# Performance work log

Measured on AMD Instinct MI355X. Metric: run time of the kernel, lower is better.

Reference implementation:

```python
import jax, jax.numpy as jnp
import numpy as np

B, T, D = 2, 2048, 1024
F_DIM = 4096
E = 8


def setup_inputs() -> dict:
    key = jax.random.key(0)
    ks = jax.random.split(key, 6)
    x = jax.random.normal(ks[0], (B, T, D), dtype=jnp.float32)
    Wr = jax.random.normal(ks[1], (E, D), dtype=jnp.float32) * 0.02  # router weight [E, D]
    W1 = jax.random.normal(ks[2], (E, F_DIM, D), dtype=jnp.float32) * 0.02  # per-expert Linear(D->F) weights
    b1 = jnp.zeros((E, F_DIM), dtype=jnp.float32)
    W2 = jax.random.normal(ks[3], (E, D, F_DIM), dtype=jnp.float32) * 0.02  # per-expert Linear(F->D) weights
    b2 = jnp.zeros((E, D), dtype=jnp.float32)
    return {"x": x, "Wr": Wr, "W1": W1, "b1": b1, "W2": W2, "b2": b2, "top_k": 2}


def reference(x, Wr, W1, b1, W2, b2, top_k):
    # router scores: [b, t, E]
    scores = jnp.einsum('btd,ed->bte', x, Wr)
    topk_vals, topk_idx = jax.lax.top_k(scores, top_k)  # [b, t, k]
    # Dense compute over all experts (E is small); grouped-GEMM equivalent of the
    # original per-token loop. hidden: [b, t, E, F]
    h = jax.nn.relu(jnp.einsum('btd,efd->btef', x, W1) + b1)
    all_out = jnp.einsum('btef,edf->bted', h, W2) + b2  # [b, t, E, D]
    # gather the top-k experts' outputs per token: [b, t, k, D]
    gathered = jnp.take_along_axis(all_out, topk_idx[..., None], axis=2)
    # FAITHFUL to source: softmax over the sequence dim (dim=-1 of [b, t]),
    # applied independently per top-k slot.
    weight = jax.nn.softmax(topk_vals, axis=1)  # [b, t, k]
    out = jnp.sum(weight[..., None] * gathered, axis=2)  # [b, t, D]
    return out
```

## Files before the change

kernel.cpp:

```cpp
#include <hip/hip_runtime.h>
#include <stdint.h>

typedef short bf16x8 __attribute__((ext_vector_type(8)));
typedef float f32x4 __attribute__((ext_vector_type(4)));

#define NTOK 4096
#define DDIM 1024
#define FDIM 4096
#define NEXP 8
#define SEQ  2048

#define FB_MAXROWS 8704
#define FB_MAXTILES 136
#define N_MAXROWS 9216
#define N_MAXTILES 72

#define GLOAD16(g, l) __builtin_amdgcn_global_load_lds( \
    (const __attribute__((address_space(1))) unsigned int*)(const void*)(g), \
    (__attribute__((address_space(3))) unsigned int*)(l), 16, 0, 0)

#define WAIT_LGKM0() asm volatile("s_waitcnt lgkmcnt(0)" ::: "memory")
#define WAIT_VM8()   asm volatile("s_waitcnt vmcnt(8)" ::: "memory")
#define WAIT_VM0()   asm volatile("s_waitcnt vmcnt(0)" ::: "memory")
#define SBAR()       __builtin_amdgcn_s_barrier()
#define SCHEDB()     __builtin_amdgcn_sched_barrier(0)

__device__ __forceinline__ unsigned short f2bf(float f) {
    union { float f; unsigned int u; } v; v.f = f;
    unsigned int u = v.u;
    unsigned int r = (u + 0x7FFFu + ((u >> 16) & 1u)) >> 16;
    return (unsigned short)r;
}
__device__ __forceinline__ unsigned int pk2(float a, float b) {
    return (unsigned int)f2bf(a) | ((unsigned int)f2bf(b) << 16);
}

__global__ __launch_bounds__(256) void cvt_kernel(
    const float* __restrict__ src, unsigned short* __restrict__ dst, int n4)
{
    int i = blockIdx.x * 256 + threadIdx.x;
    const int stride = gridDim.x * 256;
    for (; i < n4; i += stride) {
        const float4 v = ((const float4*)src)[i];
        ushort4 o;
        o.x = f2bf(v.x); o.y = f2bf(v.y); o.z = f2bf(v.z); o.w = f2bf(v.w);
        ((ushort4*)dst)[i] = o;
    }
}

__global__ __launch_bounds__(256) void router_kernel(
    const float* __restrict__ x, const float* __restrict__ Wr,
    float* __restrict__ topk_vals, int* __restrict__ topk_idx,
    int* __restrict__ counts)
{
    const int wave = threadIdx.x >> 6;
    const int lane = threadIdx.x & 63;
    const int t = blockIdx.x * 4 + wave;
    const float4* xr = (const float4*)(x + (size_t)t * DDIM);

    float acc[NEXP];
#pragma unroll
    for (int e = 0; e < NEXP; ++e) acc[e] = 0.0f;

    for (int d = lane; d < DDIM / 4; d += 64) {
        const float4 xv = xr[d];
#pragma unroll
        for (int e = 0; e < NEXP; ++e) {
            const float4 wv = ((const float4*)(Wr + e * DDIM))[d];
            acc[e] = fmaf(xv.x, wv.x, acc[e]);
            acc[e] = fmaf(xv.y, wv.y, acc[e]);
            acc[e] = fmaf(xv.z, wv.z, acc[e]);
            acc[e] = fmaf(xv.w, wv.w, acc[e]);
        }
    }
#pragma unroll
    for (int e = 0; e < NEXP; ++e) {
        for (int off = 32; off > 0; off >>= 1)
            acc[e] += __shfl_xor(acc[e], off, 64);
    }
    if (lane == 0) {
        float best = -3.4e38f, second = -3.4e38f;
        int bi = 0, si = 0;
#pragma unroll
        for (int e = 0; e < NEXP; ++e) {
            const float s = acc[e];
            if (s > best) { second = best; si = bi; best = s; bi = e; }
            else if (s > second) { second = s; si = e; }
        }
        topk_vals[t * 2 + 0] = best;
        topk_vals[t * 2 + 1] = second;
        topk_idx[t * 2 + 0] = bi;
        topk_idx[t * 2 + 1] = si;
        atomicAdd(&counts[bi], 1);
        atomicAdd(&counts[si], 1);
    }
}

__global__ __launch_bounds__(256) void softmax_seq_kernel(
    const float* __restrict__ tv, float* __restrict__ weight)
{
    const int b = blockIdx.x >> 1;
    const int k = blockIdx.x & 1;
    const float* base = tv + (size_t)b * SEQ * 2 + k;
    float* wbase = weight + (size_t)b * SEQ * 2 + k;
    __shared__ float red[256];
    const int tid = threadIdx.x;

    float m = -3.4e38f;
    for (int t = tid; t < SEQ; t += 256) m = fmaxf(m, base[t * 2]);
    red[tid] = m; __syncthreads();
    for (int s = 128; s > 0; s >>= 1) {
        if (tid < s) red[tid] = fmaxf(red[tid], red[tid + s]);
        __syncthreads();
    }
    m = red[0];
    __syncthreads();

    float sum = 0.0f;
    for (int t = tid; t < SEQ; t += 256) sum += expf(base[t * 2] - m);
    red[tid] = sum; __syncthreads();
    for (int s = 128; s > 0; s >>= 1) {
        if (tid < s) red[tid] += red[tid + s];
        __syncthreads();
    }
    const float inv = 1.0f / red[0];
    for (int t = tid; t < SEQ; t += 256)
        wbase[t * 2] = expf(base[t * 2] - m) * inv;
}

__global__ void scan_kernel(const int* __restrict__ counts,
                            int* __restrict__ padOff, int* __restrict__ cursor,
                            int padBits)
{
    if (threadIdx.x == 0) {
        const int pad = (1 << padBits) - 1;
        int o = 0;
        for (int e = 0; e < NEXP; ++e) {
            padOff[e] = o;
            o += ((counts[e] + pad) >> padBits) << padBits;
        }
        padOff[NEXP] = o;
    }
    if (threadIdx.x < NEXP) cursor[threadIdx.x] = 0;
}

__global__ __launch_bounds__(256) void scatter_kernel(
    const int* __restrict__ topk_idx, const int* __restrict__ padOff,
    int* __restrict__ cursor, int* __restrict__ perm)
{
    const int t = blockIdx.x * 256 + threadIdx.x;
#pragma unroll
    for (int k = 0; k < 2; ++k) {
        const int e = topk_idx[t * 2 + k];
        const int pos = padOff[e] + atomicAdd(&cursor[e], 1);
        perm[pos] = t * 2 + k;
    }
}


__global__ __launch_bounds__(256) void gemm1_p(
    const unsigned short* __restrict__ Xb, const unsigned short* __restrict__ Wb,
    const float* __restrict__ b1, const int* __restrict__ perm,
    const int* __restrict__ padOff, unsigned short* __restrict__ h)
{
    const int bid = blockIdx.x;
    const int swz = (bid & 7) * 288 + (bid >> 3);
    const int by = swz % N_MAXTILES;
    const int bx = swz / N_MAXTILES;
    const int row0 = by * 128;
    if (row0 >= padOff[NEXP]) return;
    int e = 0;
#pragma unroll
    for (int i = 1; i < NEXP; ++i) if (row0 >= padOff[i]) e = i;

    __shared__ unsigned short As[2][128 * 64];
    __shared__ unsigned short Bs[2][128 * 64];

    const int tid = threadIdx.x;
    const int w = tid >> 6, lane = tid & 63;
    const int wm = (w & 1) * 64, wn = (w >> 1) * 64;
    const int fr = lane & 15, kg = lane >> 4;
    const int col0 = bx * 128;

    const int gchunk = ((lane & 7) ^ (lane >> 3)) * 8;

    const unsigned short* aSrc[4];
    const unsigned short* bSrc[4];
#pragma unroll
    for (int j = 0; j < 4; ++j) {
        const int r = w * 32 + j * 8 + (lane >> 3);
        const int pm = perm[row0 + r];
        const int tok = (pm >= 0) ? (pm >> 1) : 0;
        aSrc[j] = Xb + (size_t)tok * DDIM + gchunk;
        bSrc[j] = Wb + ((size_t)e * FDIM + col0 + r) * DDIM + gchunk;
    }

    f32x4 acc[4][4] = {};

#define STAGE1(buf, koff) do { \
    for (int j = 0; j < 4; ++j) { \
        GLOAD16(aSrc[j] + (koff), &As[buf][(w * 4 + j) * 512]); \
        GLOAD16(bSrc[j] + (koff), &Bs[buf][(w * 4 + j) * 512]); \
    } } while (0)

    const int NT = DDIM / 64;
    STAGE1(0, 0);
    STAGE1(1, 64);
    SCHEDB(); WAIT_VM8(); SBAR(); SCHEDB();

    int cur = 0;
    for (int t = 0; t < NT; ++t) {
        const unsigned short* Ab = &As[cur][0];
        const unsigned short* Bb = &Bs[cur][0];
        bf16x8 a[2][4], b[2][4];
#pragma unroll
        for (int kk = 0; kk < 2; ++kk) {
#pragma unroll
            for (int m = 0; m < 4; ++m)
                a[kk][m] = *(const bf16x8*)&Ab[(wm + m * 16 + fr) * 64 + (((kk << 2) | kg) ^ (fr & 7)) * 8];
#pragma unroll
            for (int n = 0; n < 4; ++n)
                b[kk][n] = *(const bf16x8*)&Bb[(wn + n * 16 + fr) * 64 + (((kk << 2) | kg) ^ (fr & 7)) * 8];
        }
        WAIT_LGKM0(); SCHEDB();
        SBAR(); SCHEDB();
        if (t + 2 < NT) STAGE1(cur, (t + 2) * 64);
#pragma unroll
        for (int kk = 0; kk < 2; ++kk)
#pragma unroll
            for (int m = 0; m < 4; ++m)
#pragma unroll
                for (int n = 0; n < 4; ++n)
                    acc[m][n] = __builtin_amdgcn_mfma_f32_16x16x32_bf16(a[kk][m], b[kk][n], acc[m][n], 0, 0, 0);
        if (t + 1 < NT) {
            SCHEDB();
            if (t + 2 < NT) { WAIT_VM8(); } else { WAIT_VM0(); }
            SBAR(); SCHEDB();
        }
        cur ^= 1;
    }
#undef STAGE1

#pragma unroll
    for (int n = 0; n < 4; ++n) {
        const int colg = col0 + wn + n * 16 + fr;
        const float bias = b1[e * FDIM + colg];
#pragma unroll
        for (int m = 0; m < 4; ++m) {
#pragma unroll
            for (int r = 0; r < 4; ++r) {
                const int rowg = row0 + wm + m * 16 + kg * 4 + r;
                h[(size_t)rowg * FDIM + colg] = f2bf(fmaxf(acc[m][n][r] + bias, 0.0f));
            }
        }
    }
}

__global__ __launch_bounds__(256) void gemm2_p(
    const unsigned short* __restrict__ h, const unsigned short* __restrict__ Wb,
    const float* __restrict__ b2, const int* __restrict__ perm,
    const int* __restrict__ padOff, const float* __restrict__ weight,
    float* __restrict__ out)
{
    const int bid = blockIdx.x;
    const int swz = (bid & 7) * 144 + (bid >> 3);
    const int by = swz % N_MAXTILES;
    const int rest = swz / N_MAXTILES;
    const int bx = rest & 7;
    const int kc = rest >> 3;
    const int row0 = by * 128;
    if (row0 >= padOff[NEXP]) return;
    int e = 0;
#pragma unroll
    for (int i = 1; i < NEXP; ++i) if (row0 >= padOff[i]) e = i;

    __shared__ unsigned short As[2][128 * 64];
    __shared__ unsigned short Bs[2][128 * 64];

    const int tid = threadIdx.x;
    const int w = tid >> 6, lane = tid & 63;
    const int wm = (w & 1) * 64, wn = (w >> 1) * 64;
    const int fr = lane & 15, kg = lane >> 4;
    const int col0 = bx * 128;
    const int kbase = kc * (FDIM / 2);

    const int gchunk = ((lane & 7) ^ (lane >> 3)) * 8;

    const unsigned short* aSrc[4];
    const unsigned short* bSrc[4];
#pragma unroll
    for (int j = 0; j < 4; ++j) {
        const int r = w * 32 + j * 8 + (lane >> 3);
        aSrc[j] = h + (size_t)(row0 + r) * FDIM + kbase + gchunk;
        bSrc[j] = Wb + ((size_t)e * DDIM + col0 + r) * FDIM + kbase + gchunk;
    }

    f32x4 acc[4][4] = {};

#define STAGE2(buf, koff) do { \
    for (int j = 0; j < 4; ++j) { \
        GLOAD16(aSrc[j] + (koff), &As[buf][(w * 4 + j) * 512]); \
        GLOAD16(bSrc[j] + (koff), &Bs[buf][(w * 4 + j) * 512]); \
    } } while (0)

    const int NT = (FDIM / 2) / 64;
    STAGE2(0, 0);
    STAGE2(1, 64);
    SCHEDB(); WAIT_VM8(); SBAR(); SCHEDB();

    int cur = 0;
    for (int t = 0; t < NT; ++t) {
        const unsigned short* Ab = &As[cur][0];
        const unsigned short* Bb = &Bs[cur][0];
        bf16x8 a[2][4], b[2][4];
#pragma unroll
        for (int kk = 0; kk < 2; ++kk) {
#pragma unroll
            for (int m = 0; m < 4; ++m)
                a[kk][m] = *(const bf16x8*)&Ab[(wm + m * 16 + fr) * 64 + (((kk << 2) | kg) ^ (fr & 7)) * 8];
#pragma unroll
            for (int n = 0; n < 4; ++n)
                b[kk][n] = *(const bf16x8*)&Bb[(wn + n * 16 + fr) * 64 + (((kk << 2) | kg) ^ (fr & 7)) * 8];
        }
        WAIT_LGKM0(); SCHEDB();
        SBAR(); SCHEDB();
        if (t + 2 < NT) STAGE2(cur, (t + 2) * 64);
#pragma unroll
        for (int kk = 0; kk < 2; ++kk)
#pragma unroll
            for (int m = 0; m < 4; ++m)
#pragma unroll
                for (int n = 0; n < 4; ++n)
                    acc[m][n] = __builtin_amdgcn_mfma_f32_16x16x32_bf16(a[kk][m], b[kk][n], acc[m][n], 0, 0, 0);
        if (t + 1 < NT) {
            SCHEDB();
            if (t + 2 < NT) { WAIT_VM8(); } else { WAIT_VM0(); }
            SBAR(); SCHEDB();
        }
        cur ^= 1;
    }
#undef STAGE2

#pragma unroll
    for (int n = 0; n < 4; ++n) {
        const int colg = col0 + wn + n * 16 + fr;
        const float bias = (kc == 0) ? b2[e * DDIM + colg] : 0.0f;
#pragma unroll
        for (int m = 0; m < 4; ++m) {
#pragma unroll
            for (int r = 0; r < 4; ++r) {
                const int rowg = row0 + wm + m * 16 + kg * 4 + r;
                const int pm = perm[rowg];
                if (pm >= 0) {
                    const float wgt = weight[pm];
                    atomicAdd(&out[(size_t)(pm >> 1) * DDIM + colg], (acc[m][n][r] + bias) * wgt);
                }
            }
        }
    }
}


__global__ __launch_bounds__(256) void gemm1_fb(
    const float* __restrict__ x, const float* __restrict__ W1,
    const float* __restrict__ b1, const int* __restrict__ perm,
    const int* __restrict__ padOff, unsigned short* __restrict__ h)
{
    const int row0 = blockIdx.y * 64;
    if (row0 >= padOff[NEXP]) return;
    int e = 0;
#pragma unroll
    for (int i = 1; i < NEXP; ++i) if (row0 >= padOff[i]) e = i;

    __shared__ unsigned short As[64][40];
    __shared__ unsigned short Bs[64][40];

    const int tid = threadIdx.x;
    const int srow = tid >> 2;
    const int skp = (tid & 3) << 3;

    const int pm = perm[row0 + srow];
    const float* aSrc = (pm >= 0) ? (x + (size_t)(pm >> 1) * DDIM + skp) : 0;
    const int fRow = blockIdx.x * 64 + srow;
    const float* bSrc = W1 + ((size_t)e * FDIM + fRow) * DDIM + skp;

    const int lane = tid & 63;
    const int wm = ((tid >> 7) & 1) * 32;
    const int wn = ((tid >> 6) & 1) * 32;
    const int fr = lane & 15;
    const int kg = lane >> 4;

    f32x4 acc[2][2] = {{{0,0,0,0},{0,0,0,0}},{{0,0,0,0},{0,0,0,0}}};

    for (int k0 = 0; k0 < DDIM; k0 += 32) {
        uint4 av = make_uint4(0, 0, 0, 0);
        if (aSrc) {
            const float4 lo = *(const float4*)(aSrc + k0);
            const float4 hi = *(const float4*)(aSrc + k0 + 4);
            av.x = pk2(lo.x, lo.y); av.y = pk2(lo.z, lo.w);
            av.z = pk2(hi.x, hi.y); av.w = pk2(hi.z, hi.w);
        }
        const float4 bl = *(const float4*)(bSrc + k0);
        const float4 bh = *(const float4*)(bSrc + k0 + 4);
        uint4 bv;
        bv.x = pk2(bl.x, bl.y); bv.y = pk2(bl.z, bl.w);
        bv.z = pk2(bh.x, bh.y); bv.w = pk2(bh.z, bh.w);

        __syncthreads();
        *(uint4*)&As[srow][skp] = av;
        *(uint4*)&Bs[srow][skp] = bv;
        __syncthreads();

        const bf16x8 a0 = *(const bf16x8*)&As[wm + 0  + fr][kg << 3];
        const bf16x8 a1 = *(const bf16x8*)&As[wm + 16 + fr][kg << 3];
        const bf16x8 b0 = *(const bf16x8*)&Bs[wn + 0  + fr][kg << 3];
        const bf16x8 b1v = *(const bf16x8*)&Bs[wn + 16 + fr][kg << 3];
        acc[0][0] = __builtin_amdgcn_mfma_f32_16x16x32_bf16(a0, b0,  acc[0][0], 0, 0, 0);
        acc[0][1] = __builtin_amdgcn_mfma_f32_16x16x32_bf16(a0, b1v, acc[0][1], 0, 0, 0);
        acc[1][0] = __builtin_amdgcn_mfma_f32_16x16x32_bf16(a1, b0,  acc[1][0], 0, 0, 0);
        acc[1][1] = __builtin_amdgcn_mfma_f32_16x16x32_bf16(a1, b1v, acc[1][1], 0, 0, 0);
    }

#pragma unroll
    for (int mi = 0; mi < 2; ++mi)
#pragma unroll
        for (int ni = 0; ni < 2; ++ni) {
            const int colg = blockIdx.x * 64 + wn + ni * 16 + fr;
            const float bias = b1[e * FDIM + colg];
#pragma unroll
            for (int r = 0; r < 4; ++r) {
                const int rowg = row0 + wm + mi * 16 + (kg << 2) + r;
                float v = acc[mi][ni][r] + bias;
                v = fmaxf(v, 0.0f);
                h[(size_t)rowg * FDIM + colg] = f2bf(v);
            }
        }
}

__global__ __launch_bounds__(256) void gemm2_fb(
    const unsigned short* __restrict__ h, const float* __restrict__ W2,
    const float* __restrict__ b2, const int* __restrict__ perm,
    const int* __restrict__ padOff, const float* __restrict__ weight,
    float* __restrict__ out)
{
    const int row0 = blockIdx.y * 64;
    if (row0 >= padOff[NEXP]) return;
    int e = 0;
#pragma unroll
    for (int i = 1; i < NEXP; ++i) if (row0 >= padOff[i]) e = i;

    __shared__ unsigned short As[64][40];
    __shared__ unsigned short Bs[64][40];

    const int tid = threadIdx.x;
    const int srow = tid >> 2;
    const int skp = (tid & 3) << 3;

    const unsigned short* aSrc = h + (size_t)(row0 + srow) * FDIM + skp;
    const int dRow = blockIdx.x * 64 + srow;
    const float* bSrc = W2 + ((size_t)e * DDIM + dRow) * FDIM + skp;

    const int lane = tid & 63;
    const int wm = ((tid >> 7) & 1) * 32;
    const int wn = ((tid >> 6) & 1) * 32;
    const int fr = lane & 15;
    const int kg = lane >> 4;

    f32x4 acc[2][2] = {{{0,0,0,0},{0,0,0,0}},{{0,0,0,0},{0,0,0,0}}};

    for (int k0 = 0; k0 < FDIM; k0 += 32) {
        const uint4 av = *(const uint4*)(aSrc + k0);
        const float4 bl = *(const float4*)(bSrc + k0);
        const float4 bh = *(const float4*)(bSrc + k0 + 4);
        uint4 bv;
        bv.x = pk2(bl.x, bl.y); bv.y = pk2(bl.z, bl.w);
        bv.z = pk2(bh.x, bh.y); bv.w = pk2(bh.z, bh.w);

        __syncthreads();
        *(uint4*)&As[srow][skp] = av;
        *(uint4*)&Bs[srow][skp] = bv;
        __syncthreads();

        const bf16x8 a0 = *(const bf16x8*)&As[wm + 0  + fr][kg << 3];
        const bf16x8 a1 = *(const bf16x8*)&As[wm + 16 + fr][kg << 3];
        const bf16x8 b0 = *(const bf16x8*)&Bs[wn + 0  + fr][kg << 3];
        const bf16x8 b1v = *(const bf16x8*)&Bs[wn + 16 + fr][kg << 3];
        acc[0][0] = __builtin_amdgcn_mfma_f32_16x16x32_bf16(a0, b0,  acc[0][0], 0, 0, 0);
        acc[0][1] = __builtin_amdgcn_mfma_f32_16x16x32_bf16(a0, b1v, acc[0][1], 0, 0, 0);
        acc[1][0] = __builtin_amdgcn_mfma_f32_16x16x32_bf16(a1, b0,  acc[1][0], 0, 0, 0);
        acc[1][1] = __builtin_amdgcn_mfma_f32_16x16x32_bf16(a1, b1v, acc[1][1], 0, 0, 0);
    }

#pragma unroll
    for (int mi = 0; mi < 2; ++mi)
#pragma unroll
        for (int ni = 0; ni < 2; ++ni) {
            const int colg = blockIdx.x * 64 + wn + ni * 16 + fr;
            const float bias = b2[e * DDIM + colg];
#pragma unroll
            for (int r = 0; r < 4; ++r) {
                const int rowg = row0 + wm + mi * 16 + (kg << 2) + r;
                const int pm = perm[rowg];
                if (pm >= 0) {
                    const float w = weight[pm];
                    const float v = (acc[mi][ni][r] + bias) * w;
                    atomicAdd(&out[(size_t)(pm >> 1) * DDIM + colg], v);
                }
            }
        }
}

extern "C" void kernel_launch(void* const* d_in, const int* in_sizes, int n_in,
                              void* d_out, int out_size, void* d_ws, size_t ws_size,
                              hipStream_t stream)
{
    const float* x  = (const float*)d_in[0];
    const float* Wr = (const float*)d_in[1];
    const float* W1 = (const float*)d_in[2];
    const float* b1 = (const float*)d_in[3];
    const float* W2 = (const float*)d_in[4];
    const float* b2 = (const float*)d_in[5];
    float* out = (float*)d_out;
    char* ws = (char*)d_ws;

    float* topk_vals = (float*)(ws);
    float* weight    = (float*)(ws + 32768);
    int*   topk_idx  = (int*)(ws + 65536);
    int*   counts    = (int*)(ws + 98304);
    int*   padOff    = (int*)(ws + 98368);
    int*   cursor    = (int*)(ws + 98432);
    int*   perm      = (int*)(ws + 98496);

    const size_t NEED = 151257088ULL;

    if (ws_size >= NEED) {
        unsigned short* Xb = (unsigned short*)(ws + 262144);
        unsigned short* h  = (unsigned short*)(ws + 8650752);
        unsigned short* Wb = (unsigned short*)(ws + 84148224);

        hipMemsetAsync(counts, 0, NEXP * sizeof(int), stream);
        hipMemsetAsync(perm, 0xFF, N_MAXROWS * sizeof(int), stream);
        hipMemsetAsync(out, 0, (size_t)out_size * sizeof(float), stream);

        cvt_kernel<<<2048, 256, 0, stream>>>(x, Xb, NTOK * DDIM / 4);
        cvt_kernel<<<2048, 256, 0, stream>>>(W1, Wb, NEXP * FDIM * DDIM / 4);
        router_kernel<<<NTOK / 4, 256, 0, stream>>>(x, Wr, topk_vals, topk_idx, counts);
        softmax_seq_kernel<<<4, 256, 0, stream>>>(topk_vals, weight);
        scan_kernel<<<1, 64, 0, stream>>>(counts, padOff, cursor, 7);
        scatter_kernel<<<NTOK / 256, 256, 0, stream>>>(topk_idx, padOff, cursor, perm);

        gemm1_p<<<32 * N_MAXTILES, 256, 0, stream>>>(Xb, Wb, b1, perm, padOff, h);
        cvt_kernel<<<2048, 256, 0, stream>>>(W2, Wb, NEXP * DDIM * FDIM / 4);
        gemm2_p<<<16 * N_MAXTILES, 256, 0, stream>>>(h, Wb, b2, perm, padOff, weight, out);
    } else {
        unsigned short* h = (unsigned short*)(ws + 135168);

        hipMemsetAsync(counts, 0, NEXP * sizeof(int), stream);
        hipMemsetAsync(perm, 0xFF, FB_MAXROWS * sizeof(int), stream);
        hipMemsetAsync(out, 0, (size_t)out_size * sizeof(float), stream);

        router_kernel<<<NTOK / 4, 256, 0, stream>>>(x, Wr, topk_vals, topk_idx, counts);
        softmax_seq_kernel<<<4, 256, 0, stream>>>(topk_vals, weight);
        scan_kernel<<<1, 64, 0, stream>>>(counts, padOff, cursor, 6);
        scatter_kernel<<<NTOK / 256, 256, 0, stream>>>(topk_idx, padOff, cursor, perm);

        gemm1_fb<<<dim3(FDIM / 64, FB_MAXTILES), 256, 0, stream>>>(x, W1, b1, perm, padOff, h);
        gemm2_fb<<<dim3(DDIM / 64, FB_MAXTILES), 256, 0, stream>>>(h, W2, b2, perm, padOff, weight, out);
    }
}
```

Measured before the change: 524.3 us.

## Fuse fp32 weight conversion into GEMMs and replace atomic scatter with combine

The separate passes converting W1 and W2 to bf16 are removed. Each GEMM now loads fp32 weight tiles into registers, converts them to bf16 and writes them into swizzled shared memory, with the next tile prefetched into registers during compute. GEMM2 no longer splits K; it writes weighted per-slot rows to a float buffer, and a new combine kernel sums each token's two slots, replacing atomicAdd and the output memset. This saves the full read and write of both weight tensors per call, but doubles the fp32 weight bytes each GEMM reads, places conversion ALU work in the inner loop, and uses simpler synchronisation than the previous async global-to-LDS pipeline.

```diff
diff --git a/kernel.cpp b/kernel.cpp
--- a/kernel.cpp
+++ b/kernel.cpp
@@ -13,17 +13,13 @@
 #define FB_MAXROWS 8704
 #define FB_MAXTILES 136
 #define N_MAXROWS 9216
-#define N_MAXTILES 72
+#define N_MT 72
 
 #define GLOAD16(g, l) __builtin_amdgcn_global_load_lds( \
     (const __attribute__((address_space(1))) unsigned int*)(const void*)(g), \
     (__attribute__((address_space(3))) unsigned int*)(l), 16, 0, 0)
 
-#define WAIT_LGKM0() asm volatile("s_waitcnt lgkmcnt(0)" ::: "memory")
-#define WAIT_VM8()   asm volatile("s_waitcnt vmcnt(8)" ::: "memory")
-#define WAIT_VM0()   asm volatile("s_waitcnt vmcnt(0)" ::: "memory")
-#define SBAR()       __builtin_amdgcn_s_barrier()
-#define SCHEDB()     __builtin_amdgcn_sched_barrier(0)
+#define SCHEDB() __builtin_amdgcn_sched_barrier(0)
 
 __device__ __forceinline__ unsigned short f2bf(float f) {
     union { float f; unsigned int u; } v; v.f = f;
@@ -146,7 +142,7 @@
 
 __global__ __launch_bounds__(256) void scatter_kernel(
     const int* __restrict__ topk_idx, const int* __restrict__ padOff,
-    int* __restrict__ cursor, int* __restrict__ perm)
+    int* __restrict__ cursor, int* __restrict__ perm, int* __restrict__ ipos)
 {
     const int t = blockIdx.x * 256 + threadIdx.x;
 #pragma unroll
@@ -154,19 +150,20 @@
         const int e = topk_idx[t * 2 + k];
         const int pos = padOff[e] + atomicAdd(&cursor[e], 1);
         perm[pos] = t * 2 + k;
-    }
-}
-
-
-__global__ __launch_bounds__(256) void gemm1_p(
-    const unsigned short* __restrict__ Xb, const unsigned short* __restrict__ Wb,
+        ipos[t * 2 + k] = pos;
+    }
+}
+
+
+__global__ __launch_bounds__(256, 2) void gemm1_r(
+    const unsigned short* __restrict__ Xb, const float* __restrict__ W1,
     const float* __restrict__ b1, const int* __restrict__ perm,
     const int* __restrict__ padOff, unsigned short* __restrict__ h)
 {
     const int bid = blockIdx.x;
     const int swz = (bid & 7) * 288 + (bid >> 3);
-    const int by = swz % N_MAXTILES;
-    const int bx = swz / N_MAXTILES;
+    const int by = swz % N_MT;
+    const int bx = swz / N_MT;
     const int row0 = by * 128;
     if (row0 >= padOff[NEXP]) return;
     int e = 0;
@@ -183,48 +180,57 @@
     const int col0 = bx * 128;
 
     const int gchunk = ((lane & 7) ^ (lane >> 3)) * 8;
-
     const unsigned short* aSrc[4];
-    const unsigned short* bSrc[4];
 #pragma unroll
     for (int j = 0; j < 4; ++j) {
         const int r = w * 32 + j * 8 + (lane >> 3);
         const int pm = perm[row0 + r];
         const int tok = (pm >= 0) ? (pm >> 1) : 0;
         aSrc[j] = Xb + (size_t)tok * DDIM + gchunk;
-        bSrc[j] = Wb + ((size_t)e * FDIM + col0 + r) * DDIM + gchunk;
-    }
+    }
+
+    const int brow = tid >> 4;
+    const int bk4  = (tid & 15) * 4;
+    const int bc   = (tid & 15) >> 1;
+    const int rs   = brow & 7;
+    const int bsw  = (bc ^ rs) * 8 + (tid & 1) * 4;
+    const float* wSrc = W1 + ((size_t)e * FDIM + col0) * DDIM + bk4;
 
     f32x4 acc[4][4] = {};
-
-#define STAGE1(buf, koff) do { \
-    for (int j = 0; j < 4; ++j) { \
-        GLOAD16(aSrc[j] + (koff), &As[buf][(w * 4 + j) * 512]); \
-        GLOAD16(bSrc[j] + (koff), &Bs[buf][(w * 4 + j) * 512]); \
+    float4 breg[8];
+
+#define ALOAD1(buf, koff) do { _Pragma("unroll") \
+    for (int j = 0; j < 4; ++j) GLOAD16(aSrc[j] + (koff), &As[buf][(w * 4 + j) * 512]); } while (0)
+#define BLOAD1(koff) do { _Pragma("unroll") \
+    for (int j = 0; j < 8; ++j) breg[j] = *(const float4*)(wSrc + (size_t)(j * 16 + brow) * DDIM + (koff)); } while (0)
+#define BWRITE1(buf) do { _Pragma("unroll") \
+    for (int j = 0; j < 8; ++j) { \
+        const int row = j * 16 + brow; \
+        *(uint2*)&Bs[buf][row * 64 + bsw] = make_uint2(pk2(breg[j].x, breg[j].y), pk2(breg[j].z, breg[j].w)); \
     } } while (0)
 
     const int NT = DDIM / 64;
-    STAGE1(0, 0);
-    STAGE1(1, 64);
-    SCHEDB(); WAIT_VM8(); SBAR(); SCHEDB();
+    BLOAD1(0); SCHEDB();
+    ALOAD1(0, 0); SCHEDB();
+    BWRITE1(0);
+    __syncthreads();
 
     int cur = 0;
     for (int t = 0; t < NT; ++t) {
+        if (t + 1 < NT) { BLOAD1((t + 1) * 64); SCHEDB(); ALOAD1(cur ^ 1, (t + 1) * 64); SCHEDB(); }
         const unsigned short* Ab = &As[cur][0];
         const unsigned short* Bb = &Bs[cur][0];
         bf16x8 a[2][4], b[2][4];
 #pragma unroll
         for (int kk = 0; kk < 2; ++kk) {
+            const int cx = (kk << 2) | kg;
 #pragma unroll
             for (int m = 0; m < 4; ++m)
-                a[kk][m] = *(const bf16x8*)&Ab[(wm + m * 16 + fr) * 64 + (((kk << 2) | kg) ^ (fr & 7)) * 8];
+                a[kk][m] = *(const bf16x8*)&Ab[(wm + m * 16 + fr) * 64 + ((cx ^ (fr & 7)) << 3)];
 #pragma unroll
             for (int n = 0; n < 4; ++n)
-                b[kk][n] = *(const bf16x8*)&Bb[(wn + n * 16 + fr) * 64 + (((kk << 2) | kg) ^ (fr & 7)) * 8];
-        }
-        WAIT_LGKM0(); SCHEDB();
-        SBAR(); SCHEDB();
-        if (t + 2 < NT) STAGE1(cur, (t + 2) * 64);
+                b[kk][n] = *(const bf16x8*)&Bb[(wn + n * 16 + fr) * 64 + ((cx ^ (fr & 7)) << 3)];
+        }
 #pragma unroll
         for (int kk = 0; kk < 2; ++kk)
 #pragma unroll
@@ -232,14 +238,13 @@
 #pragma unroll
                 for (int n = 0; n < 4; ++n)
                     acc[m][n] = __builtin_amdgcn_mfma_f32_16x16x32_bf16(a[kk][m], b[kk][n], acc[m][n], 0, 0, 0);
-        if (t + 1 < NT) {
-            SCHEDB();
-            if (t + 2 < NT) { WAIT_VM8(); } else { WAIT_VM0(); }
-            SBAR(); SCHEDB();
-        }
+        if (t + 1 < NT) { BWRITE1(cur ^ 1); }
+        __syncthreads();
         cur ^= 1;
     }
-#undef STAGE1
+#undef ALOAD1
+#undef BLOAD1
+#undef BWRITE1
 
 #pragma unroll
     for (int n = 0; n < 4; ++n) {
@@ -256,18 +261,16 @@
     }
 }
 
-__global__ __launch_bounds__(256) void gemm2_p(
-    const unsigned short* __restrict__ h, const unsigned short* __restrict__ Wb,
+__global__ __launch_bounds__(256, 2) void gemm2_r(
+    const unsigned short* __restrict__ h, const float* __restrict__ W2,
     const float* __restrict__ b2, const int* __restrict__ perm,
     const int* __restrict__ padOff, const float* __restrict__ weight,
-    float* __restrict__ out)
+    float* __restrict__ y)
 {
     const int bid = blockIdx.x;
-    const int swz = (bid & 7) * 144 + (bid >> 3);
-    const int by = swz % N_MAXTILES;
-    const int rest = swz / N_MAXTILES;
-    const int bx = rest & 7;
-    const int kc = rest >> 3;
+    const int swz = (bid & 7) * 72 + (bid >> 3);
+    const int by = swz % N_MT;
+    const int bx = swz / N_MT;
     const int row0 = by * 128;
     if (row0 >= padOff[NEXP]) return;
     int e = 0;
@@ -282,49 +285,57 @@
     const int wm = (w & 1) * 64, wn = (w >> 1) * 64;
     const int fr = lane & 15, kg = lane >> 4;
     const int col0 = bx * 128;
-    const int kbase = kc * (FDIM / 2);
 
     const int gchunk = ((lane & 7) ^ (lane >> 3)) * 8;
-
     const unsigned short* aSrc[4];
-    const unsigned short* bSrc[4];
 #pragma unroll
     for (int j = 0; j < 4; ++j) {
         const int r = w * 32 + j * 8 + (lane >> 3);
-        aSrc[j] = h + (size_t)(row0 + r) * FDIM + kbase + gchunk;
-        bSrc[j] = Wb + ((size_t)e * DDIM + col0 + r) * FDIM + kbase + gchunk;
-    }
+        aSrc[j] = h + (size_t)(row0 + r) * FDIM + gchunk;
+    }
+
+    const int brow = tid >> 4;
+    const int bk4  = (tid & 15) * 4;
+    const int bc   = (tid & 15) >> 1;
+    const int rs   = brow & 7;
+    const int bsw  = (bc ^ rs) * 8 + (tid & 1) * 4;
+    const float* wSrc = W2 + ((size_t)e * DDIM + col0) * FDIM + bk4;
 
     f32x4 acc[4][4] = {};
-
-#define STAGE2(buf, koff) do { \
-    for (int j = 0; j < 4; ++j) { \
-        GLOAD16(aSrc[j] + (koff), &As[buf][(w * 4 + j) * 512]); \
-        GLOAD16(bSrc[j] + (koff), &Bs[buf][(w * 4 + j) * 512]); \
+    float4 breg[8];
+
+#define ALOAD2(buf, koff) do { _Pragma("unroll") \
+    for (int j = 0; j < 4; ++j) GLOAD16(aSrc[j] + (koff), &As[buf][(w * 4 + j) * 512]); } while (0)
+#define BLOAD2(koff) do { _Pragma("unroll") \
+    for (int j = 0; j < 8; ++j) breg[j] = *(const float4*)(wSrc + (size_t)(j * 16 + brow) * FDIM + (koff)); } while (0)
+#define BWRITE2(buf) do { _Pragma("unroll") \
+    for (int j = 0; j < 8; ++j) { \
+        const int row = j * 16 + brow; \
+        *(uint2*)&Bs[buf][row * 64 + bsw] = make_uint2(pk2(breg[j].x, breg[j].y), pk2(breg[j].z, breg[j].w)); \
     } } while (0)
 
-    const int NT = (FDIM / 2) / 64;
-    STAGE2(0, 0);
-    STAGE2(1, 64);
-    SCHEDB(); WAIT_VM8(); SBAR(); SCHEDB();
+    const int NT = FDIM / 64;
+    BLOAD2(0); SCHEDB();
+    ALOAD2(0, 0); SCHEDB();
+    BWRITE2(0);
+    __syncthreads();
 
     int cur = 0;
     for (int t = 0; t < NT; ++t) {
+        if (t + 1 < NT) { BLOAD2((t + 1) * 64); SCHEDB(); ALOAD2(cur ^ 1, (t + 1) * 64); SCHEDB(); }
         const unsigned short* Ab = &As[cur][0];
         const unsigned short* Bb = &Bs[cur][0];
         bf16x8 a[2][4], b[2][4];
 #pragma unroll
         for (int kk = 0; kk < 2; ++kk) {
+            const int cx = (kk << 2) | kg;
 #pragma unroll
             for (int m = 0; m < 4; ++m)
-                a[kk][m] = *(const bf16x8*)&Ab[(wm + m * 16 + fr) * 64 + (((kk << 2) | kg) ^ (fr & 7)) * 8];
+                a[kk][m] = *(const bf16x8*)&Ab[(wm + m * 16 + fr) * 64 + ((cx ^ (fr & 7)) << 3)];
 #pragma unroll
             for (int n = 0; n < 4; ++n)
-                b[kk][n] = *(const bf16x8*)&Bb[(wn + n * 16 + fr) * 64 + (((kk << 2) | kg) ^ (fr & 7)) * 8];
-        }
-        WAIT_LGKM0(); SCHEDB();
-        SBAR(); SCHEDB();
-        if (t + 2 < NT) STAGE2(cur, (t + 2) * 64);
+                b[kk][n] = *(const bf16x8*)&Bb[(wn + n * 16 + fr) * 64 + ((cx ^ (fr & 7)) << 3)];
+        }
 #pragma unroll
         for (int kk = 0; kk < 2; ++kk)
 #pragma unroll
@@ -332,19 +343,18 @@
 #pragma unroll
                 for (int n = 0; n < 4; ++n)
                     acc[m][n] = __builtin_amdgcn_mfma_f32_16x16x32_bf16(a[kk][m], b[kk][n], acc[m][n], 0, 0, 0);
-        if (t + 1 < NT) {
-            SCHEDB();
-            if (t + 2 < NT) { WAIT_VM8(); } else { WAIT_VM0(); }
-            SBAR(); SCHEDB();
-        }
+        if (t + 1 < NT) { BWRITE2(cur ^ 1); }
+        __syncthreads();
         cur ^= 1;
     }
-#undef STAGE2
+#undef ALOAD2
+#undef BLOAD2
+#undef BWRITE2
 
 #pragma unroll
     for (int n = 0; n < 4; ++n) {
         const int colg = col0 + wn + n * 16 + fr;
-        const float bias = (kc == 0) ? b2[e * DDIM + colg] : 0.0f;
+        const float bias = b2[e * DDIM + colg];
 #pragma unroll
         for (int m = 0; m < 4; ++m) {
 #pragma unroll
@@ -352,12 +362,26 @@
                 const int rowg = row0 + wm + m * 16 + kg * 4 + r;
                 const int pm = perm[rowg];
                 if (pm >= 0) {
-                    const float wgt = weight[pm];
-                    atomicAdd(&out[(size_t)(pm >> 1) * DDIM + colg], (acc[m][n][r] + bias) * wgt);
+                    y[(size_t)rowg * DDIM + colg] = (acc[m][n][r] + bias) * weight[pm];
                 }
             }
         }
     }
+}
+
+__global__ __launch_bounds__(256) void combine_kernel(
+    const float* __restrict__ y, const int* __restrict__ ipos,
+    float* __restrict__ out)
+{
+    const int t = blockIdx.x;
+    const int c = threadIdx.x;
+    const int p0 = ipos[t * 2 + 0];
+    const int p1 = ipos[t * 2 + 1];
+    const float4 v0 = ((const float4*)(y + (size_t)p0 * DDIM))[c];
+    const float4 v1 = ((const float4*)(y + (size_t)p1 * DDIM))[c];
+    float4 o;
+    o.x = v0.x + v1.x; o.y = v0.y + v1.y; o.z = v0.z + v1.z; o.w = v0.w + v1.w;
+    ((float4*)(out + (size_t)t * DDIM))[c] = o;
 }
 
 
@@ -530,30 +554,29 @@
     int*   padOff    = (int*)(ws + 98368);
     int*   cursor    = (int*)(ws + 98432);
     int*   perm      = (int*)(ws + 98496);
+    int*   ipos      = (int*)(ws + 135424);
 
     const size_t NEED = 151257088ULL;
 
     if (ws_size >= NEED) {
         unsigned short* Xb = (unsigned short*)(ws + 262144);
         unsigned short* h  = (unsigned short*)(ws + 8650752);
-        unsigned short* Wb = (unsigned short*)(ws + 84148224);
+        float*          y  = (float*)(ws + 84148224);
 
         hipMemsetAsync(counts, 0, NEXP * sizeof(int), stream);
         hipMemsetAsync(perm, 0xFF, N_MAXROWS * sizeof(int), stream);
-        hipMemsetAsync(out, 0, (size_t)out_size * sizeof(float), stream);
 
         cvt_kernel<<<2048, 256, 0, stream>>>(x, Xb, NTOK * DDIM / 4);
-        cvt_kernel<<<2048, 256, 0, stream>>>(W1, Wb, NEXP * FDIM * DDIM / 4);
         router_kernel<<<NTOK / 4, 256, 0, stream>>>(x, Wr, topk_vals, topk_idx, counts);
         softmax_seq_kernel<<<4, 256, 0, stream>>>(topk_vals, weight);
         scan_kernel<<<1, 64, 0, stream>>>(counts, padOff, cursor, 7);
-        scatter_kernel<<<NTOK / 256, 256, 0, stream>>>(topk_idx, padOff, cursor, perm);
-
-        gemm1_p<<<32 * N_MAXTILES, 256, 0, stream>>>(Xb, Wb, b1, perm, padOff, h);
-        cvt_kernel<<<2048, 256, 0, stream>>>(W2, Wb, NEXP * DDIM * FDIM / 4);
-        gemm2_p<<<16 * N_MAXTILES, 256, 0, stream>>>(h, Wb, b2, perm, padOff, weight, out);
+        scatter_kernel<<<NTOK / 256, 256, 0, stream>>>(topk_idx, padOff, cursor, perm, ipos);
+
+        gemm1_r<<<32 * N_MT, 256, 0, stream>>>(Xb, W1, b1, perm, padOff, h);
+        gemm2_r<<<8 * N_MT, 256, 0, stream>>>(h, W2, b2, perm, padOff, weight, y);
+        combine_kernel<<<NTOK, 256, 0, stream>>>(y, ipos, out);
     } else {
-        unsigned short* h = (unsigned short*)(ws + 135168);
+        unsigned short* h = (unsigned short*)(ws + 172032);
 
         hipMemsetAsync(counts, 0, NEXP * sizeof(int), stream);
         hipMemsetAsync(perm, 0xFF, FB_MAXROWS * sizeof(int), stream);
@@ -562,7 +585,7 @@
         router_kernel<<<NTOK / 4, 256, 0, stream>>>(x, Wr, topk_vals, topk_idx, counts);
         softmax_seq_kernel<<<4, 256, 0, stream>>>(topk_vals, weight);
         scan_kernel<<<1, 64, 0, stream>>>(counts, padOff, cursor, 6);
-        scatter_kernel<<<NTOK / 256, 256, 0, stream>>>(topk_idx, padOff, cursor, perm);
+        scatter_kernel<<<NTOK / 256, 256, 0, stream>>>(topk_idx, padOff, cursor, perm, ipos);
 
         gemm1_fb<<<dim3(FDIM / 64, FB_MAXTILES), 256, 0, stream>>>(x, W1, b1, perm, padOff, h);
         gemm2_fb<<<dim3(DDIM / 64, FB_MAXTILES), 256, 0, stream>>>(h, W2, b2, perm, padOff, weight, out);
```

Result: slower. 558.0 us (+6.4%).
